# Performance work log

Measured on AMD Instinct MI355X. Metric: run time of the kernel, lower is better.

Reference implementation:

```python
import jax, jax.numpy as jnp
import numpy as np

HID, NQ, NKV, HD = 4096, 32, 8, 128
EPS = 1e-6
GOLDEN = 1.618033988749895
BASE = 10000.0


def _rmsnorm(x, w, eps=EPS):
    var = jnp.mean(x.astype(jnp.float32) ** 2, axis=-1, keepdims=True)
    return (x * jax.lax.rsqrt(var + eps)).astype(x.dtype) * w


def _rope_half(t, pos, inv_freq):
    # t: (B,T,H,dh); pos: (B,T); inv_freq: (dh//2,)
    ang = pos.astype(jnp.float32)[..., None] * inv_freq  # (B,T,dq)
    cos = jnp.cos(ang)[:, :, None, :]
    sin = jnp.sin(ang)[:, :, None, :]
    dq = inv_freq.shape[0]
    t1, t2 = t[..., :dq], t[..., dq:]
    return jnp.concatenate([t1 * cos - t2 * sin, t1 * sin + t2 * cos], axis=-1)


def _apply_ggrope(q, k, row_ids, col_ids):
    # 2D RoPE: first half of head_dim encodes rows, second half encodes cols;
    # column frequencies scaled by the golden ratio (GGRoPE).
    dh = HD // 2
    inv_freq = 1.0 / (BASE ** (jnp.arange(0, dh, 2, dtype=jnp.float32) / dh))
    inv_freq_col = inv_freq * GOLDEN

    def rot(t):
        tr = _rope_half(t[..., :dh], row_ids, inv_freq)
        tc = _rope_half(t[..., dh:], col_ids, inv_freq_col)
        return jnp.concatenate([tr, tc], axis=-1)

    return rot(q), rot(k)


def setup_inputs() -> dict:
    key = jax.random.key(0)
    ks = jax.random.split(key, 9)
    B, T = 1, 2048
    s = 0.02
    return {
        "x": jax.random.normal(ks[0], (B, T, HID), jnp.float32),
        "row_ids": jax.random.randint(ks[1], (B, T), 0, 30),
        "col_ids": jax.random.randint(ks[2], (B, T), 0, 30),
        "attention_mask": jnp.zeros((B, 1, T, T), jnp.float32),
        "Wq": jax.random.normal(ks[3], (HID, NQ * HD), jnp.float32) * s,
        "Wk": jax.random.normal(ks[4], (HID, NKV * HD), jnp.float32) * s,
        "Wv": jax.random.normal(ks[5], (HID, NKV * HD), jnp.float32) * s,
        "Wo": jax.random.normal(ks[6], (NQ * HD, HID), jnp.float32) * s,
        "q_norm_w": jnp.ones((HD,), jnp.float32),
        "k_norm_w": jnp.ones((HD,), jnp.float32),
    }


def reference(x, row_ids, col_ids, attention_mask, Wq, Wk, Wv, Wo, q_norm_w, k_norm_w):
    B, T, _ = x.shape
    group = NQ // NKV
    q = (x @ Wq).reshape(B, T, NQ, HD)
    k = (x @ Wk).reshape(B, T, NKV, HD)
    v = (x @ Wv).reshape(B, T, NKV, HD)
    q = _rmsnorm(q, q_norm_w)
    k = _rmsnorm(k, k_norm_w)
    q, k = _apply_ggrope(q, k, row_ids, col_ids)
    # expand KV heads to match query heads (GQA)
    k = jnp.repeat(k, group, axis=2)  # (B,T,NQ,HD)
    v = jnp.repeat(v, group, axis=2)
    q = q.transpose(0, 2, 1, 3)  # (B,NQ,T,HD)
    k = k.transpose(0, 2, 1, 3)
    v = v.transpose(0, 2, 1, 3)
    ssmax_scale = (HD ** -0.5) * np.log(max(T, 2)).astype(np.float32)
    scores = jnp.einsum("bhqd,bhkd->bhqk", q, k) * ssmax_scale
    scores = scores + attention_mask
    attn = jax.nn.softmax(scores.astype(jnp.float32), axis=-1).astype(q.dtype)
    out = jnp.einsum("bhqk,bhkd->bhqd", attn, v)
    out = out.transpose(0, 2, 1, 3).reshape(B, T, NQ * HD)
    return out @ Wo
```

## Files before the change

kernel.cpp:

```cpp
#include <hip/hip_runtime.h>
#include <hip/hip_bf16.h>

typedef unsigned short u16;
typedef __attribute__((ext_vector_type(8))) short bf16x8;
typedef __attribute__((ext_vector_type(4))) float f32x4;

#define LOG2E_F 1.4426950408889634f
#define QSCALE (0.08838834764831845f * 7.625595228825695f * 1.4426950408889634f)

__device__ __forceinline__ u16 f2bf(float f) {
  unsigned x = __float_as_uint(f);
  unsigned r = (x + 0x7fffu + ((x >> 16) & 1u)) >> 16;
  return (u16)r;
}
__device__ __forceinline__ float bf2f(u16 u) {
  return __uint_as_float(((unsigned)u) << 16);
}
__device__ __forceinline__ float exp2a(float x) {
  float r;
  asm("v_exp_f32 %0, %1" : "=v"(r) : "v"(x));
  return r;
}
__device__ __forceinline__ unsigned cvtpk(float lo, float hi) {
  unsigned r;
  asm("v_cvt_pk_bf16_f32 %0, %1, %2" : "=v"(r) : "v"(lo), "v"(hi));
  return r;
}

__device__ __forceinline__ void gload_lds16(const void* g, void* l) {
  __builtin_amdgcn_global_load_lds(
      (__attribute__((address_space(1))) void*)(g),
      (__attribute__((address_space(3))) void*)(l), 16, 0, 0);
}

__device__ __forceinline__ f32x4 mfma16(bf16x8 a, bf16x8 b, f32x4 c) {
  return __builtin_amdgcn_mfma_f32_16x16x32_bf16(a, b, c, 0, 0, 0);
}

__global__ __launch_bounds__(256) void setup(const float* __restrict__ Wq,
                                             const float* __restrict__ Wk,
                                             const float* __restrict__ Wv,
                                             const float* __restrict__ Wo,
                                             u16* __restrict__ wqkvt,
                                             u16* __restrict__ wot,
                                             const float4* __restrict__ x,
                                             ushort4* __restrict__ xb,
                                             const float4* __restrict__ mask,
                                             int* __restrict__ flag,
                                             const int* __restrict__ row_ids,
                                             const int* __restrict__ col_ids,
                                             float4* __restrict__ trig) {
  int bid = blockIdx.x;
  int tid = threadIdx.x;
  if (bid >= 10240) {
    bid -= 10240;
    if (bid < 8192) {
      size_t i = (size_t)bid * 256 + tid;
      float4 v = x[i];
      ushort4 o;
      o.x = f2bf(v.x); o.y = f2bf(v.y); o.z = f2bf(v.z); o.w = f2bf(v.w);
      xb[i] = o;
    } else if (bid < 12288) {
      size_t i = (size_t)(bid - 8192) * 256 + tid;
      float4 v = mask[i];
      if (v.x != 0.f || v.y != 0.f || v.z != 0.f || v.w != 0.f) atomicOr(flag, 1);
    } else {
      int idx = (bid - 12288) * 256 + tid;
      int tok = idx >> 5, i = idx & 31;
      float inv = exp2f(-(float)i * 0.41524101186092030f);
      float ar = (float)row_ids[tok] * inv;
      float ac = (float)col_ids[tok] * inv * 1.618033988749895f;
      float4 o;
      o.x = cosf(ar); o.y = sinf(ar); o.z = cosf(ac); o.w = sinf(ac);
      trig[idx] = o;
    }
    return;
  }
  __shared__ float t[64][65];
  const float* src;
  u16* dst;
  int N;
  if (bid < 4096)      { src = Wq; dst = wqkvt;                       N = 4096; }
  else if (bid < 5120) { src = Wk; dst = wqkvt + (size_t)4096 * 4096; N = 1024; bid -= 4096; }
  else if (bid < 6144) { src = Wv; dst = wqkvt + (size_t)5120 * 4096; N = 1024; bid -= 5120; }
  else                 { src = Wo; dst = wot;                         N = 4096; bid -= 6144; }
  int kt = bid & 63, nt = bid >> 6;
  int k0 = kt * 64, n0 = nt * 64;
#pragma unroll
  for (int it = 0; it < 16; ++it) {
    int idx = it * 256 + tid;
    int row = idx >> 6, col = idx & 63;
    t[row][col] = src[(size_t)(k0 + row) * N + n0 + col];
  }
  __syncthreads();
#pragma unroll
  for (int it = 0; it < 8; ++it) {
    int idx = it * 256 + tid;
    int nrow = idx >> 5, kc = idx & 31;
    ushort2 o;
    o.x = f2bf(t[kc * 2][nrow]);
    o.y = f2bf(t[kc * 2 + 1][nrow]);
    *(ushort2*)&dst[(size_t)(n0 + nrow) * 4096 + k0 + kc * 2] = o;
  }
}

__global__ __launch_bounds__(256) void rope_kernel(u16* __restrict__ qk,
                                                   const float4* __restrict__ trig,
                                                   const float* __restrict__ qw,
                                                   const float* __restrict__ kw) {
  const int tok = blockIdx.x;
  const int tid = threadIdx.x;
  const int w = tid >> 6, lane = tid & 63;
  float4 t4 = trig[tok * 32 + (lane & 31)];
  float sgn = (lane < 32) ? -1.0f : 1.0f;

  for (int it = 0; it < 10; ++it) {
    int hh = w + it * 4;
    bool isQ = (hh < 32);
    int colbase = isQ ? hh * 128 : 4096 + (hh - 32) * 128;
    const float* nw = isQ ? qw : kw;
    float scale = isQ ? QSCALE : 1.0f;
    u16* p = qk + (size_t)tok * 5120 + colbase;
    float v1 = bf2f(p[lane]);
    float v2 = bf2f(p[64 + lane]);
    float w1 = nw[lane], w2 = nw[64 + lane];
    float ss = v1 * v1 + v2 * v2;
    ss += __shfl_xor(ss, 1);  ss += __shfl_xor(ss, 2);  ss += __shfl_xor(ss, 4);
    ss += __shfl_xor(ss, 8);  ss += __shfl_xor(ss, 16); ss += __shfl_xor(ss, 32);
    float rinv = rsqrtf(ss * (1.0f / 128.0f) + 1e-6f);
    float n1 = v1 * rinv * w1;
    float n2 = v2 * rinv * w2;
    float p1 = __shfl_xor(n1, 32);
    float p2 = __shfl_xor(n2, 32);
    float r1 = n1 * t4.x + sgn * p1 * t4.y;
    float r2 = n2 * t4.z + sgn * p2 * t4.w;
    p[lane]      = f2bf(r1 * scale);
    p[64 + lane] = f2bf(r2 * scale);
  }
}

template <int MODE>
__global__ __launch_bounds__(512, 2) void gemm256(const u16* __restrict__ A,
                                                  const u16* __restrict__ Bt,
                                                  void* __restrict__ C0,
                                                  u16* __restrict__ Vt, int nnt) {
  extern __shared__ char smem[];
  const int tid = threadIdx.x, lane = tid & 63, w = tid >> 6;
  const int l15 = lane & 15, l4 = lane >> 4;
  const int wr = w >> 2, wc = w & 3;
  constexpr int NF = (MODE == 0) ? 3 : 4;
  constexpr int BNW = (MODE == 0) ? 48 : 64;

  int wgid = (blockIdx.x & 7) * (gridDim.x >> 3) + (blockIdx.x >> 3);
  int kh = 0;
  if (MODE == 1) { kh = wgid >> 7; wgid &= 127; }
  const int mt = wgid / nnt, nt = wgid % nnt;
  const int m0 = mt * 256;
  const int n0 = nt * ((MODE == 0) ? 192 : 256);
  const int tbase = kh * 32;

  const int kswz = (((tid & 7) ^ ((tid >> 3) & 7)) << 4);
  const char* arow = (const char*)A + (size_t)(m0 + (tid >> 3)) * 8192 + kswz;
  const char* brow = (const char*)Bt + (size_t)(n0 + (tid >> 3)) * 8192 + kswz;

  auto stageA = [&](int t, int h) {
#pragma unroll
    for (int rd = 0; rd < 2; ++rd)
      gload_lds16(arow + (size_t)(h * 128 + rd * 64) * 8192 + t * 128,
                  smem + ((t & 1) * 2 + h) * 16384 + rd * 8192 + w * 1024);
  };
  auto stageB0 = [&](int t) {
#pragma unroll
    for (int rd = 0; rd < 3; ++rd)
      gload_lds16(brow + (size_t)(rd * 64) * 8192 + t * 128,
                  smem + 65536 + (t & 1) * 24576 + rd * 8192 + w * 1024);
  };
  auto stageB1 = [&](int t, int h) {
#pragma unroll
    for (int rd = 0; rd < 2; ++rd)
      gload_lds16(brow + (size_t)(h * 128 + rd * 64) * 8192 + t * 128,
                  smem + 65536 + ((t & 1) * 2 + h) * 16384 + rd * 8192 + w * 1024);
  };

  f32x4 acc[8][NF];
#pragma unroll
  for (int i = 0; i < 8; ++i)
#pragma unroll
    for (int j = 0; j < NF; ++j) acc[i][j] = (f32x4){0.f, 0.f, 0.f, 0.f};

  const int aoff0 = ((l4) ^ (l15 & 7)) << 4;
  const int aoff1 = ((4 + l4) ^ (l15 & 7)) << 4;

  stageA(tbase, 0); stageA(tbase, 1);
  if constexpr (MODE == 0) {
    stageB0(tbase); stageB0(tbase + 1);
    asm volatile("s_waitcnt vmcnt(3)" ::: "memory");
  } else {
    stageB1(tbase, 0); stageB1(tbase, 1);
    stageB1(tbase + 1, 0); stageB1(tbase + 1, 1);
    asm volatile("s_waitcnt vmcnt(4)" ::: "memory");
  }
  __builtin_amdgcn_s_barrier();

  auto do_iter = [&](int t0, int last) {
    bf16x8 bfr[NF][2];
#pragma unroll
    for (int p = 0; p < 8; ++p) {
      const int s = p >> 2, qd = p & 3;
      const char* aT = smem + (s * 2 + wr) * 16384 + l15 * 128;
      bf16x8 afr[2][2];
#pragma unroll
      for (int jm = 0; jm < 2; ++jm) {
        afr[jm][0] = *(const bf16x8*)(aT + (2 * qd + jm) * 2048 + aoff0);
        afr[jm][1] = *(const bf16x8*)(aT + (2 * qd + jm) * 2048 + aoff1);
      }
      if (qd == 0) {
        const char* bT;
        if constexpr (MODE == 0)
          bT = smem + 65536 + s * 24576 + (wc * 48 + l15) * 128;
        else
          bT = smem + 65536 + (s * 2 + (wc >> 1)) * 16384 +
               ((wc & 1) * 64 + l15) * 128;
#pragma unroll
        for (int nf = 0; nf < NF; ++nf) {
          bfr[nf][0] = *(const bf16x8*)(bT + nf * 2048 + aoff0);
          bfr[nf][1] = *(const bf16x8*)(bT + nf * 2048 + aoff1);
        }
      }
      if (p == 0) { stageA(t0 + 1, 0); stageA(t0 + 1, 1); }
      if (!last) {
        if constexpr (MODE == 0) {
          if (p == 1) stageB0(t0 + 2);
          if (p == 5) stageB0(t0 + 3);
        } else {
          if (p == 1) stageB1(t0 + 2, 0);
          if (p == 2) stageB1(t0 + 2, 1);
          if (p == 5) stageB1(t0 + 3, 0);
          if (p == 6) stageB1(t0 + 3, 1);
        }
        if (p == 4) { stageA(t0 + 2, 0); stageA(t0 + 2, 1); }
      }
      if (p == 3) {
        if (last) asm volatile("s_waitcnt vmcnt(0)" ::: "memory");
        else if constexpr (MODE == 0)
          asm volatile("s_waitcnt vmcnt(3)" ::: "memory");
        else
          asm volatile("s_waitcnt vmcnt(4)" ::: "memory");
      }
      if (p == 7 && !last) {
        if constexpr (MODE == 0)
          asm volatile("s_waitcnt vmcnt(3)" ::: "memory");
        else
          asm volatile("s_waitcnt vmcnt(4)" ::: "memory");
      }
      __builtin_amdgcn_s_barrier();
      asm volatile("s_waitcnt lgkmcnt(0)" ::: "memory");
      __builtin_amdgcn_sched_barrier(0);
      __builtin_amdgcn_s_setprio(1);
#pragma unroll
      for (int ks = 0; ks < 2; ++ks)
#pragma unroll
        for (int jm = 0; jm < 2; ++jm)
#pragma unroll
          for (int nf = 0; nf < NF; ++nf)
            acc[2 * qd + jm][nf] =
                mfma16(afr[jm][ks], bfr[nf][ks], acc[2 * qd + jm][nf]);
      __builtin_amdgcn_s_setprio(0);
      __builtin_amdgcn_s_barrier();
    }
  };

  constexpr int NIT = (MODE == 0) ? 32 : 16;
  for (int j = 0; j < NIT - 1; ++j) do_iter(tbase + 2 * j, 0);
  do_iter(tbase + 2 * (NIT - 1), 1);

  if (MODE == 0) {
    u16* qkp = (u16*)C0;
#pragma unroll
    for (int mf = 0; mf < 8; ++mf)
#pragma unroll
      for (int nf = 0; nf < NF; ++nf) {
        int ng = n0 + wc * BNW + nf * 16 + l15;
        if (ng < 5120) {
#pragma unroll
          for (int r = 0; r < 4; ++r) {
            int mg = m0 + wr * 128 + mf * 16 + l4 * 4 + r;
            qkp[(size_t)mg * 5120 + ng] = f2bf(acc[mf][nf][r]);
          }
        } else {
          int vr = ng - 5120;
          int mg = m0 + wr * 128 + mf * 16 + l4 * 4;
          ushort4 pk;
          pk.x = f2bf(acc[mf][nf][0]); pk.y = f2bf(acc[mf][nf][1]);
          pk.z = f2bf(acc[mf][nf][2]); pk.w = f2bf(acc[mf][nf][3]);
          *(ushort4*)&Vt[(size_t)vr * 2048 + mg] = pk;
        }
      }
  } else {
    float* Cp = (float*)C0 + (size_t)kh * 8388608;
#pragma unroll
    for (int mf = 0; mf < 8; ++mf)
#pragma unroll
      for (int nf = 0; nf < NF; ++nf) {
        int ng = n0 + wc * BNW + nf * 16 + l15;
#pragma unroll
        for (int r = 0; r < 4; ++r) {
          int mg = m0 + wr * 128 + mf * 16 + l4 * 4 + r;
          Cp[(size_t)mg * 4096 + ng] = acc[mf][nf][r];
        }
      }
  }
}

__global__ __launch_bounds__(256) void reduce2(const float4* __restrict__ p0,
                                               const float4* __restrict__ p1,
                                               float4* __restrict__ out) {
  size_t i = (size_t)blockIdx.x * 256 + threadIdx.x;
  float4 a = p0[i], b = p1[i];
  float4 o;
  o.x = a.x + b.x; o.y = a.y + b.y; o.z = a.z + b.z; o.w = a.w + b.w;
  out[i] = o;
}

__global__ __launch_bounds__(256, 2) void attn_kernel(const u16* __restrict__ qk,
                                                      const u16* __restrict__ vt,
                                                      u16* __restrict__ oat,
                                                      const float* __restrict__ mask,
                                                      const int* __restrict__ flag) {
  __shared__ u16 k_lds[2][64 * 128];
  __shared__ u16 v_lds[2][64 * 128];

  const int tid = threadIdx.x, lane = tid & 63, w = tid >> 6;
  const int l15 = lane & 15, l4 = lane >> 4;
  const int bid = blockIdx.x;
  const int hk = bid & 7;
  const int rest = bid >> 3;
  const int h = hk * 4 + (rest & 3);
  const int qt = rest >> 2;
  const int qbase = qt * 128 + w * 32;

  const bool use_mask = (*flag != 0);
  const char* kbase = (const char*)qk + 8192 + (size_t)hk * 256;
  const char* vbase = (const char*)vt + (size_t)hk * 128 * 4096;

  bf16x8 qf[2][4];
#pragma unroll
  for (int qg = 0; qg < 2; ++qg) {
    const char* qp = (const char*)qk +
                     (size_t)(qbase + qg * 16 + l15) * 10240 + h * 256 + l4 * 16;
#pragma unroll
    for (int ks = 0; ks < 4; ++ks) qf[qg][ks] = *(const bf16x8*)(qp + ks * 64);
  }

  f32x4 oacc[2][8];
#pragma unroll
  for (int qg = 0; qg < 2; ++qg)
#pragma unroll
    for (int fd = 0; fd < 8; ++fd) oacc[qg][fd] = (f32x4){0.f, 0.f, 0.f, 0.f};
  float m_run[2] = {-1e30f, -1e30f};
  float l_run[2] = {0.f, 0.f};

  int koff[4], voff[2];
#pragma unroll
  for (int ks = 0; ks < 4; ++ks) koff[ks] = ((4 * ks + l4) ^ l15) << 4;
#pragma unroll
  for (int ks = 0; ks < 2; ++ks) voff[ks] = ((4 * ks + l4) ^ (l15 & 7)) << 4;

#define STAGE(buf, kv0)                                                        \
  {                                                                            \
    _Pragma("unroll") for (int rd = 0; rd < 4; ++rd) {                         \
      int c = rd * 256 + tid;                                                  \
      int row = c >> 4;                                                        \
      int src = ((c & 15) ^ (row & 15)) << 4;                                  \
      gload_lds16(kbase + (size_t)((kv0) + row) * 10240 + src,                 \
                  (char*)k_lds[buf] + (rd * 256 + w * 64) * 16);               \
      int rowv = c >> 3;                                                       \
      int srcv = ((c & 7) ^ (rowv & 7)) << 4;                                  \
      gload_lds16(vbase + (size_t)rowv * 4096 + (kv0) * 2 + srcv,              \
                  (char*)v_lds[buf] + (rd * 256 + w * 64) * 16);               \
    }                                                                          \
  }

  STAGE(0, 0);
  asm volatile("s_waitcnt vmcnt(0)" ::: "memory");
  __builtin_amdgcn_s_barrier();
  __builtin_amdgcn_sched_barrier(0);

  for (int kt = 0; kt < 32; ++kt) {
    const int cur = kt & 1;
    const int kv0 = kt * 64;
    if (kt < 31) STAGE(cur ^ 1, kv0 + 64);

    f32x4 sA[2][4];
#pragma unroll
    for (int qg = 0; qg < 2; ++qg)
#pragma unroll
      for (int f = 0; f < 4; ++f) sA[qg][f] = (f32x4){0.f, 0.f, 0.f, 0.f};

    __builtin_amdgcn_s_setprio(1);
#pragma unroll
    for (int ks = 0; ks < 4; ++ks) {
      bf16x8 kfr[4];
#pragma unroll
      for (int f = 0; f < 4; ++f)
        kfr[f] = *(const bf16x8*)((const char*)k_lds[cur] +
                                  (16 * f + l15) * 256 + koff[ks]);
#pragma unroll
      for (int f = 0; f < 4; ++f) {
        sA[0][f] = mfma16(kfr[f], qf[0][ks], sA[0][f]);
        sA[1][f] = mfma16(kfr[f], qf[1][ks], sA[1][f]);
      }
    }
    __builtin_amdgcn_s_setprio(0);

    if (use_mask) {
#pragma unroll
      for (int qg = 0; qg < 2; ++qg) {
        int qglob = qbase + qg * 16 + l15;
#pragma unroll
        for (int f = 0; f < 4; ++f)
#pragma unroll
          for (int r = 0; r < 4; ++r) {
            int kvglob = kv0 + 16 * f + 4 * l4 + r;
            sA[qg][f][r] += LOG2E_F * mask[(size_t)qglob * 2048 + kvglob];
          }
      }
    }

    unsigned paw[2][2][4];
#pragma unroll
    for (int qg = 0; qg < 2; ++qg) {
      float mx = fmaxf(fmaxf(fmaxf(sA[qg][0][0], sA[qg][0][1]),
                             fmaxf(sA[qg][0][2], sA[qg][0][3])),
                       fmaxf(fmaxf(sA[qg][1][0], sA[qg][1][1]),
                             fmaxf(sA[qg][1][2], sA[qg][1][3])));
      float mx2 = fmaxf(fmaxf(fmaxf(sA[qg][2][0], sA[qg][2][1]),
                              fmaxf(sA[qg][2][2], sA[qg][2][3])),
                        fmaxf(fmaxf(sA[qg][3][0], sA[qg][3][1]),
                              fmaxf(sA[qg][3][2], sA[qg][3][3])));
      mx = fmaxf(mx, mx2);
      mx = fmaxf(mx, __shfl_xor(mx, 16));
      mx = fmaxf(mx, __shfl_xor(mx, 32));
      if (__any(mx > m_run[qg] + 8.0f)) {
        float mnew = fmaxf(m_run[qg], mx);
        float a = exp2a(m_run[qg] - mnew);
        l_run[qg] *= a;
        m_run[qg] = mnew;
        float a0 = __shfl(a, 4 * l4 + 0);
        float a1 = __shfl(a, 4 * l4 + 1);
        float a2 = __shfl(a, 4 * l4 + 2);
        float a3 = __shfl(a, 4 * l4 + 3);
#pragma unroll
        for (int fd = 0; fd < 8; ++fd) {
          oacc[qg][fd][0] *= a0; oacc[qg][fd][1] *= a1;
          oacc[qg][fd][2] *= a2; oacc[qg][fd][3] *= a3;
        }
      }
      float ps = 0.f;
      unsigned W[4][2];
#pragma unroll
      for (int f = 0; f < 4; ++f) {
        float p0 = exp2a(sA[qg][f][0] - m_run[qg]);
        float p1 = exp2a(sA[qg][f][1] - m_run[qg]);
        float p2 = exp2a(sA[qg][f][2] - m_run[qg]);
        float p3 = exp2a(sA[qg][f][3] - m_run[qg]);
        ps += (p0 + p1) + (p2 + p3);
        W[f][0] = cvtpk(p0, p1);
        W[f][1] = cvtpk(p2, p3);
      }
      ps += __shfl_xor(ps, 16);
      ps += __shfl_xor(ps, 32);
      l_run[qg] += ps;
#pragma unroll
      for (int ks = 0; ks < 2; ++ks)
#pragma unroll
        for (int wd = 0; wd < 4; ++wd) {
          int src = l15 + 16 * (2 * (l4 & 1) + (wd >> 1));
          unsigned v0 = (unsigned)__shfl((int)W[2 * ks][wd & 1], src);
          unsigned v1 = (unsigned)__shfl((int)W[2 * ks + 1][wd & 1], src);
          paw[qg][ks][wd] = (l4 & 2) ? v1 : v0;
        }
    }

    __builtin_amdgcn_s_setprio(1);
#pragma unroll
    for (int ks = 0; ks < 2; ++ks) {
      union { unsigned u[4]; bf16x8 v; } pa0, pa1;
#pragma unroll
      for (int wd = 0; wd < 4; ++wd) {
        pa0.u[wd] = paw[0][ks][wd];
        pa1.u[wd] = paw[1][ks][wd];
      }
#pragma unroll
      for (int fd = 0; fd < 8; ++fd) {
        bf16x8 vb = *(const bf16x8*)((const char*)v_lds[cur] +
                                     (16 * fd + l15) * 128 + voff[ks]);
        oacc[0][fd] = mfma16(pa0.v, vb, oacc[0][fd]);
        oacc[1][fd] = mfma16(pa1.v, vb, oacc[1][fd]);
      }
    }
    __builtin_amdgcn_s_setprio(0);

    if (kt < 31) {
      asm volatile("s_waitcnt vmcnt(0)" ::: "memory");
      __builtin_amdgcn_s_barrier();
      __builtin_amdgcn_sched_barrier(0);
    }
  }

#pragma unroll
  for (int qg = 0; qg < 2; ++qg) {
    float inv[4];
#pragma unroll
    for (int r = 0; r < 4; ++r) inv[r] = 1.0f / __shfl(l_run[qg], 4 * l4 + r);
#pragma unroll
    for (int fd = 0; fd < 8; ++fd) {
      int dg = h * 128 + 16 * fd + l15;
#pragma unroll
      for (int r = 0; r < 4; ++r) {
        int qrow = qbase + qg * 16 + 4 * l4 + r;
        oat[(size_t)qrow * 4096 + dg] = f2bf(oacc[qg][fd][r] * inv[r]);
      }
    }
  }
#undef STAGE
}

extern "C" void kernel_launch(void* const* d_in, const int* in_sizes, int n_in,
                              void* d_out, int out_size, void* d_ws, size_t ws_size,
                              hipStream_t stream) {
  const float* x = (const float*)d_in[0];
  const int* row_ids = (const int*)d_in[1];
  const int* col_ids = (const int*)d_in[2];
  const float* mask = (const float*)d_in[3];
  const float* Wq = (const float*)d_in[4];
  const float* Wk = (const float*)d_in[5];
  const float* Wv = (const float*)d_in[6];
  const float* Wo = (const float*)d_in[7];
  const float* qw = (const float*)d_in[8];
  const float* kw = (const float*)d_in[9];

  char* ws = (char*)d_ws;
  u16* xb      = (u16*)(ws);
  u16* wqkvt   = (u16*)(ws + 16777216);
  u16* wot     = (u16*)(ws + 67108864);
  u16* qkbuf   = (u16*)(ws + 100663296);
  u16* vtbuf   = (u16*)(ws + 121634816);
  u16* oat     = (u16*)(ws + 125829120);
  float4* trig = (float4*)(ws + 142606336);
  int* flag    = (int*)(ws + 143654912);
  float* pbuf  = (float*)(ws);

  hipFuncSetAttribute((const void*)gemm256<0>,
                      hipFuncAttributeMaxDynamicSharedMemorySize, 131072);
  hipFuncSetAttribute((const void*)gemm256<1>,
                      hipFuncAttributeMaxDynamicSharedMemorySize, 131072);

  hipMemsetAsync(flag, 0, 4, stream);
  setup<<<22784, 256, 0, stream>>>(Wq, Wk, Wv, Wo, wqkvt, wot,
                                   (const float4*)x, (ushort4*)xb,
                                   (const float4*)mask, flag, row_ids, col_ids,
                                   trig);
  gemm256<0><<<256, 512, 114688, stream>>>(xb, wqkvt, (void*)qkbuf, vtbuf, 32);
  rope_kernel<<<2048, 256, 0, stream>>>(qkbuf, trig, qw, kw);
  attn_kernel<<<512, 256, 0, stream>>>(qkbuf, vtbuf, oat, mask, flag);
  gemm256<1><<<256, 512, 131072, stream>>>(oat, wot, (void*)pbuf, nullptr, 16);
  reduce2<<<8192, 256, 0, stream>>>((const float4*)pbuf,
                                    (const float4*)(pbuf + 8388608),
                                    (float4*)d_out);
}
```

Measured before the change: 344.5 us.

## Replace split-K output GEMM with 128x128 tiles writing directly to output

The output projection GEMM no longer splits K into two halves written to a partial buffer and summed by a separate reduce kernel. It uses 128x128 tiles over the full K range across 512 workgroups and writes the result straight to the output, with smaller LDS use and a higher occupancy bound. This removes the reduce launch and the fp32 partial-buffer round trip through memory. In exchange, each tile reuses less data per load and each workgroup runs a K loop twice as long.

Measured after the change: 350.5 us. Within noise of the previous version (+1.7%).

```diff
diff --git a/kernel.cpp b/kernel.cpp
--- a/kernel.cpp
+++ b/kernel.cpp
@@ -140,66 +140,70 @@
 }
 
 template <int MODE>
-__global__ __launch_bounds__(512, 2) void gemm256(const u16* __restrict__ A,
-                                                  const u16* __restrict__ Bt,
-                                                  void* __restrict__ C0,
-                                                  u16* __restrict__ Vt, int nnt) {
+__global__ __launch_bounds__(512, (MODE == 0) ? 2 : 4)
+void gemm256(const u16* __restrict__ A, const u16* __restrict__ Bt,
+             void* __restrict__ C0, u16* __restrict__ Vt, int nnt) {
   extern __shared__ char smem[];
   const int tid = threadIdx.x, lane = tid & 63, w = tid >> 6;
   const int l15 = lane & 15, l4 = lane >> 4;
   const int wr = w >> 2, wc = w & 3;
-  constexpr int NF = (MODE == 0) ? 3 : 4;
-  constexpr int BNW = (MODE == 0) ? 48 : 64;
+  constexpr int NF = (MODE == 0) ? 3 : 2;
+  constexpr int BNW = (MODE == 0) ? 48 : 32;
+  constexpr int AHALF = (MODE == 0) ? 16384 : 8192;
+  constexpr int BOFF = (MODE == 0) ? 65536 : 32768;
+  constexpr int BSLOT = (MODE == 0) ? 24576 : 16384;
+  constexpr int NVM = (MODE == 0) ? 3 : 2;
 
   int wgid = (blockIdx.x & 7) * (gridDim.x >> 3) + (blockIdx.x >> 3);
-  int kh = 0;
-  if (MODE == 1) { kh = wgid >> 7; wgid &= 127; }
   const int mt = wgid / nnt, nt = wgid % nnt;
-  const int m0 = mt * 256;
-  const int n0 = nt * ((MODE == 0) ? 192 : 256);
-  const int tbase = kh * 32;
+  const int m0 = mt * ((MODE == 0) ? 256 : 128);
+  const int n0 = nt * ((MODE == 0) ? 192 : 128);
 
   const int kswz = (((tid & 7) ^ ((tid >> 3) & 7)) << 4);
   const char* arow = (const char*)A + (size_t)(m0 + (tid >> 3)) * 8192 + kswz;
   const char* brow = (const char*)Bt + (size_t)(n0 + (tid >> 3)) * 8192 + kswz;
 
   auto stageA = [&](int t, int h) {
-#pragma unroll
-    for (int rd = 0; rd < 2; ++rd)
-      gload_lds16(arow + (size_t)(h * 128 + rd * 64) * 8192 + t * 128,
-                  smem + ((t & 1) * 2 + h) * 16384 + rd * 8192 + w * 1024);
+    if constexpr (MODE == 0) {
+#pragma unroll
+      for (int rd = 0; rd < 2; ++rd)
+        gload_lds16(arow + (size_t)(h * 128 + rd * 64) * 8192 + t * 128,
+                    smem + ((t & 1) * 2 + h) * AHALF + rd * 8192 + w * 1024);
+    } else {
+      gload_lds16(arow + (size_t)(h * 64) * 8192 + t * 128,
+                  smem + ((t & 1) * 2 + h) * AHALF + w * 1024);
+    }
   };
-  auto stageB0 = [&](int t) {
-#pragma unroll
-    for (int rd = 0; rd < 3; ++rd)
-      gload_lds16(brow + (size_t)(rd * 64) * 8192 + t * 128,
-                  smem + 65536 + (t & 1) * 24576 + rd * 8192 + w * 1024);
+  auto stageB = [&](int t) {
+    if constexpr (MODE == 0) {
+#pragma unroll
+      for (int rd = 0; rd < 3; ++rd)
+        gload_lds16(brow + (size_t)(rd * 64) * 8192 + t * 128,
+                    smem + BOFF + (t & 1) * BSLOT + rd * 8192 + w * 1024);
+    } else {
+#pragma unroll
+      for (int rd = 0; rd < 2; ++rd)
+        gload_lds16(brow + (size_t)(rd * 64) * 8192 + t * 128,
+                    smem + BOFF + (t & 1) * BSLOT + rd * 8192 + w * 1024);
+    }
   };
-  auto stageB1 = [&](int t, int h) {
-#pragma unroll
-    for (int rd = 0; rd < 2; ++rd)
-      gload_lds16(brow + (size_t)(h * 128 + rd * 64) * 8192 + t * 128,
-                  smem + 65536 + ((t & 1) * 2 + h) * 16384 + rd * 8192 + w * 1024);
-  };
-
-  f32x4 acc[8][NF];
-#pragma unroll
-  for (int i = 0; i < 8; ++i)
+
+  constexpr int MF = (MODE == 0) ? 8 : 4;
+  f32x4 acc[MF][NF];
+#pragma unroll
+  for (int i = 0; i < MF; ++i)
 #pragma unroll
     for (int j = 0; j < NF; ++j) acc[i][j] = (f32x4){0.f, 0.f, 0.f, 0.f};
 
   const int aoff0 = ((l4) ^ (l15 & 7)) << 4;
   const int aoff1 = ((4 + l4) ^ (l15 & 7)) << 4;
 
-  stageA(tbase, 0); stageA(tbase, 1);
-  if constexpr (MODE == 0) {
-    stageB0(tbase); stageB0(tbase + 1);
+  stageA(0, 0); stageA(0, 1);
+  stageB(0); stageB(1);
+  if constexpr (MODE == 0)
     asm volatile("s_waitcnt vmcnt(3)" ::: "memory");
-  } else {
-    stageB1(tbase, 0); stageB1(tbase, 1);
-    stageB1(tbase + 1, 0); stageB1(tbase + 1, 1);
-    asm volatile("s_waitcnt vmcnt(4)" ::: "memory");
-  }
+  else
+    asm volatile("s_waitcnt vmcnt(2)" ::: "memory");
   __builtin_amdgcn_s_barrier();
 
   auto do_iter = [&](int t0, int last) {
@@ -207,20 +211,20 @@
 #pragma unroll
     for (int p = 0; p < 8; ++p) {
       const int s = p >> 2, qd = p & 3;
-      const char* aT = smem + (s * 2 + wr) * 16384 + l15 * 128;
-      bf16x8 afr[2][2];
-#pragma unroll
-      for (int jm = 0; jm < 2; ++jm) {
-        afr[jm][0] = *(const bf16x8*)(aT + (2 * qd + jm) * 2048 + aoff0);
-        afr[jm][1] = *(const bf16x8*)(aT + (2 * qd + jm) * 2048 + aoff1);
+      const char* aT = smem + (s * 2 + wr) * AHALF + l15 * 128;
+      bf16x8 afr[(MODE == 0) ? 2 : 1][2];
+      if constexpr (MODE == 0) {
+#pragma unroll
+        for (int jm = 0; jm < 2; ++jm) {
+          afr[jm][0] = *(const bf16x8*)(aT + (2 * qd + jm) * 2048 + aoff0);
+          afr[jm][1] = *(const bf16x8*)(aT + (2 * qd + jm) * 2048 + aoff1);
+        }
+      } else {
+        afr[0][0] = *(const bf16x8*)(aT + qd * 2048 + aoff0);
+        afr[0][1] = *(const bf16x8*)(aT + qd * 2048 + aoff1);
       }
       if (qd == 0) {
-        const char* bT;
-        if constexpr (MODE == 0)
-          bT = smem + 65536 + s * 24576 + (wc * 48 + l15) * 128;
-        else
-          bT = smem + 65536 + (s * 2 + (wc >> 1)) * 16384 +
-               ((wc & 1) * 64 + l15) * 128;
+        const char* bT = smem + BOFF + s * BSLOT + (wc * BNW + l15) * 128;
 #pragma unroll
         for (int nf = 0; nf < NF; ++nf) {
           bfr[nf][0] = *(const bf16x8*)(bT + nf * 2048 + aoff0);
@@ -229,55 +233,48 @@
       }
       if (p == 0) { stageA(t0 + 1, 0); stageA(t0 + 1, 1); }
       if (!last) {
-        if constexpr (MODE == 0) {
-          if (p == 1) stageB0(t0 + 2);
-          if (p == 5) stageB0(t0 + 3);
-        } else {
-          if (p == 1) stageB1(t0 + 2, 0);
-          if (p == 2) stageB1(t0 + 2, 1);
-          if (p == 5) stageB1(t0 + 3, 0);
-          if (p == 6) stageB1(t0 + 3, 1);
-        }
+        if (p == 1) stageB(t0 + 2);
         if (p == 4) { stageA(t0 + 2, 0); stageA(t0 + 2, 1); }
+        if (p == 5) stageB(t0 + 3);
       }
       if (p == 3) {
         if (last) asm volatile("s_waitcnt vmcnt(0)" ::: "memory");
-        else if constexpr (MODE == 0)
-          asm volatile("s_waitcnt vmcnt(3)" ::: "memory");
-        else
-          asm volatile("s_waitcnt vmcnt(4)" ::: "memory");
-      }
-      if (p == 7 && !last) {
-        if constexpr (MODE == 0)
-          asm volatile("s_waitcnt vmcnt(3)" ::: "memory");
-        else
-          asm volatile("s_waitcnt vmcnt(4)" ::: "memory");
-      }
+        else      asm volatile("s_waitcnt vmcnt(%0)" ::"i"(NVM): "memory");
+      }
+      if (p == 7 && !last)
+        asm volatile("s_waitcnt vmcnt(%0)" ::"i"(NVM): "memory");
       __builtin_amdgcn_s_barrier();
       asm volatile("s_waitcnt lgkmcnt(0)" ::: "memory");
       __builtin_amdgcn_sched_barrier(0);
       __builtin_amdgcn_s_setprio(1);
-#pragma unroll
-      for (int ks = 0; ks < 2; ++ks)
-#pragma unroll
-        for (int jm = 0; jm < 2; ++jm)
+      if constexpr (MODE == 0) {
+#pragma unroll
+        for (int ks = 0; ks < 2; ++ks)
+#pragma unroll
+          for (int jm = 0; jm < 2; ++jm)
+#pragma unroll
+            for (int nf = 0; nf < NF; ++nf)
+              acc[2 * qd + jm][nf] =
+                  mfma16(afr[jm][ks], bfr[nf][ks], acc[2 * qd + jm][nf]);
+      } else {
+#pragma unroll
+        for (int ks = 0; ks < 2; ++ks)
 #pragma unroll
           for (int nf = 0; nf < NF; ++nf)
-            acc[2 * qd + jm][nf] =
-                mfma16(afr[jm][ks], bfr[nf][ks], acc[2 * qd + jm][nf]);
+            acc[qd][nf] = mfma16(afr[0][ks], bfr[nf][ks], acc[qd][nf]);
+      }
       __builtin_amdgcn_s_setprio(0);
       __builtin_amdgcn_s_barrier();
     }
   };
 
-  constexpr int NIT = (MODE == 0) ? 32 : 16;
-  for (int j = 0; j < NIT - 1; ++j) do_iter(tbase + 2 * j, 0);
-  do_iter(tbase + 2 * (NIT - 1), 1);
+  for (int j = 0; j < 31; ++j) do_iter(2 * j, 0);
+  do_iter(62, 1);
 
   if (MODE == 0) {
     u16* qkp = (u16*)C0;
 #pragma unroll
-    for (int mf = 0; mf < 8; ++mf)
+    for (int mf = 0; mf < MF; ++mf)
 #pragma unroll
       for (int nf = 0; nf < NF; ++nf) {
         int ng = n0 + wc * BNW + nf * 16 + l15;
@@ -297,29 +294,19 @@
         }
       }
   } else {
-    float* Cp = (float*)C0 + (size_t)kh * 8388608;
-#pragma unroll
-    for (int mf = 0; mf < 8; ++mf)
+    float* Cp = (float*)C0;
+#pragma unroll
+    for (int mf = 0; mf < MF; ++mf)
 #pragma unroll
       for (int nf = 0; nf < NF; ++nf) {
         int ng = n0 + wc * BNW + nf * 16 + l15;
 #pragma unroll
         for (int r = 0; r < 4; ++r) {
-          int mg = m0 + wr * 128 + mf * 16 + l4 * 4 + r;
+          int mg = m0 + wr * 64 + mf * 16 + l4 * 4 + r;
           Cp[(size_t)mg * 4096 + ng] = acc[mf][nf][r];
         }
       }
   }
-}
-
-__global__ __launch_bounds__(256) void reduce2(const float4* __restrict__ p0,
-                                               const float4* __restrict__ p1,
-                                               float4* __restrict__ out) {
-  size_t i = (size_t)blockIdx.x * 256 + threadIdx.x;
-  float4 a = p0[i], b = p1[i];
-  float4 o;
-  o.x = a.x + b.x; o.y = a.y + b.y; o.z = a.z + b.z; o.w = a.w + b.w;
-  out[i] = o;
 }
 
 __global__ __launch_bounds__(256, 2) void attn_kernel(const u16* __restrict__ qk,
@@ -549,7 +536,6 @@
   u16* oat     = (u16*)(ws + 125829120);
   float4* trig = (float4*)(ws + 142606336);
   int* flag    = (int*)(ws + 143654912);
-  float* pbuf  = (float*)(ws);
 
   hipFuncSetAttribute((const void*)gemm256<0>,
                       hipFuncAttributeMaxDynamicSharedMemorySize, 131072);
@@ -564,8 +550,5 @@
   gemm256<0><<<256, 512, 114688, stream>>>(xb, wqkvt, (void*)qkbuf, vtbuf, 32);
   rope_kernel<<<2048, 256, 0, stream>>>(qkbuf, trig, qw, kw);
   attn_kernel<<<512, 256, 0, stream>>>(qkbuf, vtbuf, oat, mask, flag);
-  gemm256<1><<<256, 512, 131072, stream>>>(oat, wot, (void*)pbuf, nullptr, 16);
-  reduce2<<<8192, 256, 0, stream>>>((const float4*)pbuf,
-                                    (const float4*)(pbuf + 8388608),
-                                    (float4*)d_out);
-}
+  gemm256<1><<<512, 512, 65536, stream>>>(oat, wot, d_out, nullptr, 32);
+}
```
